# Performance work log

Hardware: AMD Instinct MI355X
Metric: run time of the kernel (lower is better)

The kernel has to match this reference:

```python
import jax, jax.numpy as jnp
import numpy as np

H, D = 16, 64  # head_num, head_dim
SCALE = 1.0 / D ** 0.5


def setup_inputs() -> dict:
    key = jax.random.key(0)
    ks = jax.random.split(key, 12)
    S, T, B, E = 2048, 2048, 2, 1024  # dec_seq, enc_seq, bs, input_dim
    return {
        "inputs": jax.random.normal(ks[0], (S, B, E), jnp.float32),
        "pos_embedding": jax.random.normal(ks[1], (T, 1, E), jnp.float32),
        "encoder_hidden_states": jax.random.normal(ks[2], (T, B, E), jnp.float32),
        "u": jax.random.normal(ks[3], (H, D), jnp.float32) * 0.02,
        "v": jax.random.normal(ks[4], (H, D), jnp.float32) * 0.02,
        "mask": jnp.zeros((S, T, 1), jnp.bool_),
        "Wkv": jax.random.normal(ks[5], (E, 2 * H * D), jnp.float32) * (E ** -0.5),
        "bkv": jnp.zeros((2 * H * D,), jnp.float32),
        "Wq": jax.random.normal(ks[6], (E, H * D), jnp.float32) * (E ** -0.5),
        "bq": jnp.zeros((H * D,), jnp.float32),
        "Wp": jax.random.normal(ks[7], (H * D, E), jnp.float32) * ((H * D) ** -0.5),
        "bp": jnp.zeros((E,), jnp.float32),
    }


def reference(inputs, pos_embedding, encoder_hidden_states, u, v, mask,
              Wkv, bkv, Wq, bq, Wp, bp):
    S, B, E = inputs.shape
    T = encoder_hidden_states.shape[0]
    # projections (fc_block == Linear)
    kv = encoder_hidden_states @ Wkv + bkv            # (T, B, 2HD)
    k, val = jnp.split(kv, 2, axis=-1)
    k = k.reshape(T, B, H, D)
    val = val.reshape(T, B, H, D)
    q = (inputs @ Wq + bq).reshape(S, B, H, D)
    q_u = q + u                                       # content bias (H, D) broadcast
    # content attention: (B, H, S, T)
    attn = jnp.einsum('sbhd,tbhd->bhst', q_u, k) * SCALE
    # mask (S, T, 1) -> (1, 1, S, T); all-False mask == original skip branch
    m = jnp.transpose(mask, (2, 0, 1))[:, None]
    attn = jnp.where(m, -jnp.inf, attn)
    attn = jax.nn.softmax(attn, axis=-1)
    # dropout is identity (eval)
    attn_vec = jnp.einsum('bhst,tbhd->sbhd', attn, val).reshape(S, B, H * D)
    return attn_vec @ Wp + bp                         # (S, B, E)
```

## Files before the change

kernel.cpp:

```cpp
#include <hip/hip_runtime.h>

#define Hh 16
#define Dd 64
#define Ss 2048
#define Tt 2048
#define Bb 2
#define Ee 1024
#define HD 1024
#define QSCALE 0.18033688011112042f

typedef __attribute__((ext_vector_type(8))) __bf16 bf16x8;
typedef __attribute__((ext_vector_type(4))) float f32x4;
typedef __attribute__((ext_vector_type(8))) unsigned short ushort8;
typedef __attribute__((ext_vector_type(2))) unsigned uint2v;

static __device__ __forceinline__ unsigned short f2b(float x) {
    union { float f; unsigned u; } v; v.f = x;
    unsigned r = v.u + 0x7FFFu + ((v.u >> 16) & 1u);
    return (unsigned short)(r >> 16);
}

static __device__ __forceinline__ unsigned cvtpk(float a, float b) {
    unsigned r;
    __asm__("v_cvt_pk_bf16_f32 %0, %1, %2" : "=v"(r) : "v"(a), "v"(b));
    return r;
}

static __device__ __forceinline__ void gld16(const unsigned short* g, unsigned short* l) {
    __builtin_amdgcn_global_load_lds(
        (const __attribute__((address_space(1))) unsigned int*)g,
        (__attribute__((address_space(3))) unsigned int*)l, 16, 0, 0);
}

static __device__ __forceinline__ void xquad(unsigned& a, unsigned& b) {
    uint2v r1 = __builtin_amdgcn_permlane32_swap(a, b, false, false);
    uint2v r2 = __builtin_amdgcn_permlane16_swap(r1[0], r1[1], false, false);
    a = r2[0]; b = r2[1];
}

static __device__ __forceinline__ bf16x8 packp(unsigned w0, unsigned w1,
                                               unsigned w2, unsigned w3) {
    union { unsigned u[4]; bf16x8 v; } x;
    x.u[0] = w0; x.u[1] = w1; x.u[2] = w2; x.u[3] = w3;
    return x.v;
}

static __device__ __forceinline__ void mkP(f32x4 s[4], bf16x8& pa0, bf16x8& pa1) {
#pragma unroll
    for (int jt = 0; jt < 4; jt++)
#pragma unroll
        for (int r = 0; r < 4; r++) s[jt][r] = __builtin_amdgcn_exp2f(s[jt][r]);
    unsigned a0 = cvtpk(s[0][0], s[0][1]), a1 = cvtpk(s[0][2], s[0][3]);
    unsigned b0 = cvtpk(s[1][0], s[1][1]), b1 = cvtpk(s[1][2], s[1][3]);
    unsigned c0 = cvtpk(s[2][0], s[2][1]), c1 = cvtpk(s[2][2], s[2][3]);
    unsigned d0 = cvtpk(s[3][0], s[3][1]), d1 = cvtpk(s[3][2], s[3][3]);
    xquad(a0, b0);
    xquad(a1, b1);
    xquad(c0, d0);
    xquad(c1, d1);
    pa0 = packp(a0, a1, b0, b1);
    pa1 = packp(c0, c1, d0, d1);
}

__global__ __launch_bounds__(256) void prep(
    const float* __restrict__ enc, const float* __restrict__ inp,
    unsigned short* __restrict__ encb, unsigned short* __restrict__ inpb,
    const float* __restrict__ Wkv, const float* __restrict__ Wq, const float* __restrict__ Wp,
    unsigned short* __restrict__ Wkvt, unsigned short* __restrict__ Wqt,
    unsigned short* __restrict__ Wpt)
{
    __shared__ float tile[64][65];
    const int bx = blockIdx.x;
    const int tid = threadIdx.x;
    if (bx < 8192) {
        const int n4each = (Tt * Bb * Ee) / 4;
        int i = bx * 256 + tid;
        const float4* src; ushort4* dst; int j;
        if (i < n4each) { src = (const float4*)enc; dst = (ushort4*)encb; j = i; }
        else            { src = (const float4*)inp; dst = (ushort4*)inpb; j = i - n4each; }
        float4 v = src[j];
        ushort4 o; o.x = f2b(v.x); o.y = f2b(v.y); o.z = f2b(v.z); o.w = f2b(v.w);
        dst[j] = o;
        return;
    }
    int u = bx - 8192;
    const float* in; unsigned short* out; int C, cblk, rblk;
    if (u < 512)       { in = Wkv; out = Wkvt; C = 2048; cblk = u & 31; rblk = u >> 5; }
    else if (u < 768)  { int v = u - 512; in = Wq; out = Wqt; C = 1024; cblk = v & 15; rblk = v >> 4; }
    else               { int v = u - 768; in = Wp; out = Wpt; C = 1024; cblk = v & 15; rblk = v >> 4; }
    const int R = 1024;
    int c0 = cblk * 64, r0 = rblk * 64;
    int tx = tid & 63, ty = tid >> 6;
    for (int i = ty; i < 64; i += 4)
        tile[i][tx] = in[(r0 + i) * (long)C + c0 + tx];
    __syncthreads();
    int c_local = tid >> 2, g = tid & 3;
    ushort8 o0, o1;
#pragma unroll
    for (int k = 0; k < 8; k++) o0[k] = f2b(tile[g * 16 + k][c_local]);
#pragma unroll
    for (int k = 0; k < 8; k++) o1[k] = f2b(tile[g * 16 + 8 + k][c_local]);
    unsigned short* dst = &out[(c0 + c_local) * (long)R + r0 + g * 16];
    *(ushort8*)dst = o0;
    *(ushort8*)(dst + 8) = o1;
}

static __device__ __forceinline__ void gemm_core(
    const unsigned short* __restrict__ A, const unsigned short* __restrict__ Bt,
    int m0, int n0, unsigned short* lA, unsigned short* lB, f32x4 acc[4][4])
{
    const int tid = threadIdx.x;
    const int lane = tid & 63;
    const int wid = tid >> 6;
    const int waveM = (wid & 1) * 64, waveN = (wid >> 1) * 64;
    const int quad = lane >> 4, low = lane & 15;
#pragma unroll
    for (int i = 0; i < 4; i++)
#pragma unroll
        for (int j = 0; j < 4; j++) acc[i][j] = (f32x4)0.0f;

    for (int k0 = 0; k0 < 1024; k0 += 32) {
        __syncthreads();
        {
            int r0 = tid >> 2, s0 = tid & 3;
            int f1 = tid + 256, r1 = f1 >> 2, s1 = f1 & 3;
            gld16(&A[(m0 + r0) * 1024 + k0 + s0 * 8], &lA[tid * 8]);
            gld16(&A[(m0 + r1) * 1024 + k0 + s1 * 8], &lA[f1 * 8]);
            gld16(&Bt[(n0 + r0) * 1024 + k0 + s0 * 8], &lB[tid * 8]);
            gld16(&Bt[(n0 + r1) * 1024 + k0 + s1 * 8], &lB[f1 * 8]);
        }
        __syncthreads();
        bf16x8 af[4], bfr[4];
#pragma unroll
        for (int i = 0; i < 4; i++)
            af[i] = *(const bf16x8*)&lA[(waveM + i * 16 + low) * 32 + quad * 8];
#pragma unroll
        for (int j = 0; j < 4; j++)
            bfr[j] = *(const bf16x8*)&lB[(waveN + j * 16 + low) * 32 + quad * 8];
#pragma unroll
        for (int i = 0; i < 4; i++)
#pragma unroll
            for (int j = 0; j < 4; j++)
                acc[i][j] = __builtin_amdgcn_mfma_f32_16x16x32_bf16(af[i], bfr[j], acc[i][j], 0, 0, 0);
    }
}

__global__ __launch_bounds__(256) void gemm12(
    const unsigned short* __restrict__ encb, const unsigned short* __restrict__ Wkvt,
    const float* __restrict__ bkv,
    const unsigned short* __restrict__ inpb, const unsigned short* __restrict__ Wqt,
    const float* __restrict__ bq, const float* __restrict__ u,
    unsigned short* __restrict__ Kw, unsigned short* __restrict__ Vb,
    unsigned short* __restrict__ qw)
{
    __shared__ unsigned short smem[128 * 130];
    unsigned short* lA = smem;
    unsigned short* lB = smem + 128 * 32;
    const int bx = blockIdx.x;
    int z, m0, n0;
    const unsigned short *Ap, *Bp;
    if (bx < 512) { z = 0; m0 = (bx >> 4) * 128; n0 = (bx & 15) * 128; Ap = encb; Bp = Wkvt; }
    else { z = 1; int i = bx - 512; m0 = (i >> 3) * 128; n0 = (i & 7) * 128; Ap = inpb; Bp = Wqt; }
    f32x4 acc[4][4];
    gemm_core(Ap, Bp, m0, n0, lA, lB, acc);
    __syncthreads();

    const int lane = threadIdx.x & 63;
    const int wid = threadIdx.x >> 6;
    const int waveM = (wid & 1) * 64, waveN = (wid >> 1) * 64;
    const int quad = lane >> 4, low = lane & 15;
#pragma unroll
    for (int i = 0; i < 4; i++)
#pragma unroll
        for (int j = 0; j < 4; j++)
#pragma unroll
            for (int r = 0; r < 4; r++) {
                int lm = waveM + i * 16 + quad * 4 + r;
                int ln = waveN + j * 16 + low;
                int gn = n0 + ln;
                float val = acc[i][j][r];
                if (z == 0) val += bkv[gn];
                else        val = (val + bq[gn] + u[gn]) * QSCALE;
                smem[lm * 130 + ln] = f2b(val);
            }
    __syncthreads();

    const int tid = threadIdx.x;
    if (z == 0 && n0 >= 1024) {
        int d = tid & 63, hp = (tid >> 6) & 1, b = tid >> 7;
        int h = ((n0 - 1024) >> 6) + hp;
        int tb = m0 >> 7;
        unsigned short* dst = &Vb[((((b << 4) | h) * 32 + tb) * 64 + d) * 64];
#pragma unroll
        for (int c = 0; c < 8; c++) {
            ushort8 o;
#pragma unroll
            for (int k = 0; k < 8; k++)
                o[k] = smem[((c * 8 + k) * 2 + b) * 130 + hp * 64 + d];
            *(ushort8*)(dst + c * 8) = o;
        }
    } else {
        int gl = tid & 127, hp = tid >> 7;
        int gm = m0 + gl;
        int t = gm >> 1, b = gm & 1;
        int h = (n0 >> 6) + hp;
        unsigned short* base = (z == 0) ? Kw : qw;
        unsigned short* dst = &base[(((b << 4) | h) * 2048 + t) * 64];
        const unsigned short* src = &smem[gl * 130 + hp * 64];
#pragma unroll
        for (int c = 0; c < 8; c++) {
            ushort8 o;
#pragma unroll
            for (int k = 0; k < 8; k++) o[k] = src[c * 8 + k];
            *(ushort8*)(dst + c * 8) = o;
        }
    }
}

__global__ __launch_bounds__(256) void gemm3(
    const unsigned short* __restrict__ av, const unsigned short* __restrict__ Wpt,
    const float* __restrict__ bp, float* __restrict__ out)
{
    __shared__ unsigned short lA[128 * 32];
    __shared__ unsigned short lB[64 * 32];
    const int tid = threadIdx.x;
    const int lane = tid & 63;
    const int wid = tid >> 6;
    const int waveM = (wid & 1) * 64, waveN = (wid >> 1) * 32;
    const int m0 = blockIdx.y * 128, n0 = blockIdx.x * 64;
    const int quad = lane >> 4, low = lane & 15;

    f32x4 acc[4][2];
#pragma unroll
    for (int i = 0; i < 4; i++)
#pragma unroll
        for (int j = 0; j < 2; j++) acc[i][j] = (f32x4)0.0f;

    for (int k0 = 0; k0 < 1024; k0 += 32) {
        __syncthreads();
        {
            int r0 = tid >> 2, s0 = tid & 3;
            int f1 = tid + 256, r1 = f1 >> 2, s1 = f1 & 3;
            gld16(&av[(m0 + r0) * 1024 + k0 + s0 * 8], &lA[tid * 8]);
            gld16(&av[(m0 + r1) * 1024 + k0 + s1 * 8], &lA[f1 * 8]);
            gld16(&Wpt[(n0 + r0) * 1024 + k0 + s0 * 8], &lB[tid * 8]);
        }
        __syncthreads();
        bf16x8 af[4], bfr[2];
#pragma unroll
        for (int i = 0; i < 4; i++)
            af[i] = *(const bf16x8*)&lA[(waveM + i * 16 + low) * 32 + quad * 8];
#pragma unroll
        for (int j = 0; j < 2; j++)
            bfr[j] = *(const bf16x8*)&lB[(waveN + j * 16 + low) * 32 + quad * 8];
#pragma unroll
        for (int i = 0; i < 4; i++)
#pragma unroll
            for (int j = 0; j < 2; j++)
                acc[i][j] = __builtin_amdgcn_mfma_f32_16x16x32_bf16(af[i], bfr[j], acc[i][j], 0, 0, 0);
    }
#pragma unroll
    for (int i = 0; i < 4; i++)
#pragma unroll
        for (int j = 0; j < 2; j++)
#pragma unroll
            for (int r = 0; r < 4; r++) {
                int gm = m0 + waveM + i * 16 + quad * 4 + r;
                int gn = n0 + waveN + j * 16 + low;
                out[gm * 1024 + gn] = acc[i][j][r] + bp[gn];
            }
}

__global__ __launch_bounds__(512, 4) void attn_kernel(
    const unsigned short* __restrict__ qw, const unsigned short* __restrict__ Kw,
    const unsigned short* __restrict__ Vb, unsigned short* __restrict__ av)
{
    __shared__ unsigned short kl[128 * 64];
    __shared__ unsigned short vt[2][64 * 64];
    const int tid = threadIdx.x;
    const int lane = tid & 63;
    const int w = tid >> 6;
    const int quad = lane >> 4, low = lane & 15;
    const int swz = low & 7;
    const int bh = blockIdx.x & 31;
    const int s0 = (blockIdx.x >> 5) * 128;
    const int s_wave = s0 + w * 16;

    bf16x8 qf0, qf1;
    {
        const unsigned short* qa = &qw[(bh * 2048 + s_wave + low) * 64];
        qf0 = *(const bf16x8*)&qa[quad * 8];
        qf1 = *(const bf16x8*)&qa[32 + quad * 8];
    }
    bf16x8 ones;
    {
        ushort8 o1;
#pragma unroll
        for (int i = 0; i < 8; i++) o1[i] = 0x3F80;
        ones = *(bf16x8*)&o1;
    }
    f32x4 o[4];
    f32x4 l_acc = (f32x4)0.0f;
#pragma unroll
    for (int j = 0; j < 4; j++) o[j] = (f32x4)0.0f;

#pragma unroll
    for (int i = 0; i < 2; i++) {
        int fl = tid + i * 512;
        int row = fl >> 3, seg = fl & 7;
        gld16(&Kw[(bh * 2048 + row) * 64 + ((seg ^ (row & 7)) << 3)], &kl[fl * 8]);
    }
    __builtin_amdgcn_sched_barrier(0);

    for (int t0 = 0; t0 < 2048; t0 += 128) {
#pragma unroll
        for (int i = 0; i < 2; i++) {
            int c2 = tid + i * 512;
            int win = c2 >> 9, inner = c2 & 511;
            int dd = inner >> 3, seg = inner & 7;
            gld16(&Vb[((bh * 32 + (t0 >> 6) + win) * 64 + dd) * 64 + ((seg ^ (dd & 7)) << 3)],
                  &vt[win][inner * 8]);
        }
        __asm__ volatile("s_waitcnt vmcnt(2)" ::: "memory");
        __builtin_amdgcn_s_barrier();
        __builtin_amdgcn_sched_barrier(0);

        f32x4 s0v[4], s1v[4];
        __builtin_amdgcn_s_setprio(1);
#pragma unroll
        for (int jt = 0; jt < 4; jt++) {
            int r = jt * 16 + low;
            bf16x8 kb0 = *(const bf16x8*)&kl[r * 64 + ((quad ^ swz) << 3)];
            bf16x8 kb1 = *(const bf16x8*)&kl[r * 64 + (((quad ^ 4) ^ swz) << 3)];
            f32x4 a = (f32x4)0.0f;
            a = __builtin_amdgcn_mfma_f32_16x16x32_bf16(kb0, qf0, a, 0, 0, 0);
            s0v[jt] = __builtin_amdgcn_mfma_f32_16x16x32_bf16(kb1, qf1, a, 0, 0, 0);
        }
        __builtin_amdgcn_s_setprio(0);
        bf16x8 p00, p01;
        mkP(s0v, p00, p01);

        __builtin_amdgcn_s_setprio(1);
#pragma unroll
        for (int jt = 0; jt < 4; jt++) {
            int r = 64 + jt * 16 + low;
            bf16x8 kb0 = *(const bf16x8*)&kl[r * 64 + ((quad ^ swz) << 3)];
            bf16x8 kb1 = *(const bf16x8*)&kl[r * 64 + (((quad ^ 4) ^ swz) << 3)];
            f32x4 a = (f32x4)0.0f;
            a = __builtin_amdgcn_mfma_f32_16x16x32_bf16(kb0, qf0, a, 0, 0, 0);
            s1v[jt] = __builtin_amdgcn_mfma_f32_16x16x32_bf16(kb1, qf1, a, 0, 0, 0);
        }
        __builtin_amdgcn_s_setprio(0);
        bf16x8 p10, p11;
        mkP(s1v, p10, p11);

        __asm__ volatile("s_waitcnt vmcnt(0)" ::: "memory");
        __builtin_amdgcn_s_barrier();
        __builtin_amdgcn_sched_barrier(0);

        {
            int tn = (t0 + 128) & 2047;
#pragma unroll
            for (int i = 0; i < 2; i++) {
                int fl = tid + i * 512;
                int row = fl >> 3, seg = fl & 7;
                gld16(&Kw[(bh * 2048 + tn + row) * 64 + ((seg ^ (row & 7)) << 3)],
                      &kl[fl * 8]);
            }
        }
        __builtin_amdgcn_sched_barrier(0);

        __builtin_amdgcn_s_setprio(1);
        l_acc = __builtin_amdgcn_mfma_f32_16x16x32_bf16(p00, ones, l_acc, 0, 0, 0);
        l_acc = __builtin_amdgcn_mfma_f32_16x16x32_bf16(p01, ones, l_acc, 0, 0, 0);
#pragma unroll
        for (int j = 0; j < 4; j++) {
            int dr = j * 16 + low;
            bf16x8 vb0 = *(const bf16x8*)&vt[0][dr * 64 + ((quad ^ swz) << 3)];
            bf16x8 vb1 = *(const bf16x8*)&vt[0][dr * 64 + (((quad ^ 4) ^ swz) << 3)];
            o[j] = __builtin_amdgcn_mfma_f32_16x16x32_bf16(p00, vb0, o[j], 0, 0, 0);
            o[j] = __builtin_amdgcn_mfma_f32_16x16x32_bf16(p01, vb1, o[j], 0, 0, 0);
        }
        l_acc = __builtin_amdgcn_mfma_f32_16x16x32_bf16(p10, ones, l_acc, 0, 0, 0);
        l_acc = __builtin_amdgcn_mfma_f32_16x16x32_bf16(p11, ones, l_acc, 0, 0, 0);
#pragma unroll
        for (int j = 0; j < 4; j++) {
            int dr = j * 16 + low;
            bf16x8 vb0 = *(const bf16x8*)&vt[1][dr * 64 + ((quad ^ swz) << 3)];
            bf16x8 vb1 = *(const bf16x8*)&vt[1][dr * 64 + (((quad ^ 4) ^ swz) << 3)];
            o[j] = __builtin_amdgcn_mfma_f32_16x16x32_bf16(p10, vb0, o[j], 0, 0, 0);
            o[j] = __builtin_amdgcn_mfma_f32_16x16x32_bf16(p11, vb1, o[j], 0, 0, 0);
        }
        __builtin_amdgcn_s_setprio(0);

        __builtin_amdgcn_s_barrier();
        __builtin_amdgcn_sched_barrier(0);
    }

    int b = bh >> 4, hh = bh & 15;
#pragma unroll
    for (int j = 0; j < 4; j++) {
#pragma unroll
        for (int r = 0; r < 4; r++) {
            int sA_ = s_wave + quad * 4 + r;
            int d = j * 16 + low;
            av[(sA_ * 2 + b) * 1024 + hh * 64 + d] = f2b(o[j][r] / l_acc[r]);
        }
    }
}

extern "C" void kernel_launch(void* const* d_in, const int* in_sizes, int n_in,
                              void* d_out, int out_size, void* d_ws, size_t ws_size,
                              hipStream_t stream)
{
    const float* inputs = (const float*)d_in[0];
    const float* enc    = (const float*)d_in[2];
    const float* u      = (const float*)d_in[3];
    const float* Wkv    = (const float*)d_in[6];
    const float* bkv    = (const float*)d_in[7];
    const float* Wq     = (const float*)d_in[8];
    const float* bq     = (const float*)d_in[9];
    const float* Wp     = (const float*)d_in[10];
    const float* bp     = (const float*)d_in[11];
    float* out = (float*)d_out;

    char* ws = (char*)d_ws;
    unsigned short* enc_b = (unsigned short*)(ws + (0ull << 20));
    unsigned short* inp_b = (unsigned short*)(ws + (8ull << 20));
    unsigned short* Wkv_t = (unsigned short*)(ws + (16ull << 20));
    unsigned short* Wq_t  = (unsigned short*)(ws + (20ull << 20));
    unsigned short* Wp_t  = (unsigned short*)(ws + (22ull << 20));
    unsigned short* Kw    = (unsigned short*)(ws + (24ull << 20));
    unsigned short* Vb    = (unsigned short*)(ws + (32ull << 20));
    unsigned short* qw    = (unsigned short*)(ws + (40ull << 20));
    unsigned short* av    = (unsigned short*)(ws + (48ull << 20));

    prep<<<8192 + 1024, 256, 0, stream>>>(enc, inputs, enc_b, inp_b, Wkv, Wq, Wp,
                                          Wkv_t, Wq_t, Wp_t);
    gemm12<<<768, 256, 0, stream>>>(enc_b, Wkv_t, bkv, inp_b, Wq_t, bq, u, Kw, Vb, qw);
    attn_kernel<<<512, 512, 0, stream>>>(qw, Kw, Vb, av);
    gemm3<<<dim3(16, 32), 256, 0, stream>>>(av, Wp_t, bp, out);
}
```

Measured before the change: 224.8 us.

## Double-buffer LDS tiles in projection GEMMs to overlap loads with MFMA

The projection GEMMs (gemm12 and gemm3) now use two LDS buffers, prefetching the next K-slice via direct global-to-LDS loads while MFMAs consume the current slice. This replaces the two barriers per iteration with one explicit waitcnt plus barrier, hiding global load latency behind compute. It doubles the LDS tile footprint in gemm3, which may reduce occupancy, and it relies on hand-placed waitcnt and sched_barrier for correctness.

Result: slower. 233.7 us (+4.0%).

```diff
diff --git a/kernel.cpp b/kernel.cpp
--- a/kernel.cpp
+++ b/kernel.cpp
@@ -107,29 +107,41 @@
 
 static __device__ __forceinline__ void gemm_core(
     const unsigned short* __restrict__ A, const unsigned short* __restrict__ Bt,
-    int m0, int n0, unsigned short* lA, unsigned short* lB, f32x4 acc[4][4])
+    int m0, int n0, unsigned short* sA, unsigned short* sB, f32x4 acc[4][4])
 {
     const int tid = threadIdx.x;
     const int lane = tid & 63;
     const int wid = tid >> 6;
     const int waveM = (wid & 1) * 64, waveN = (wid >> 1) * 64;
     const int quad = lane >> 4, low = lane & 15;
+    const int r0 = tid >> 2, s0 = tid & 3;
+    const int f1 = tid + 256, r1 = f1 >> 2, s1 = f1 & 3;
 #pragma unroll
     for (int i = 0; i < 4; i++)
 #pragma unroll
         for (int j = 0; j < 4; j++) acc[i][j] = (f32x4)0.0f;
 
+    gld16(&A[(m0 + r0) * 1024 + s0 * 8], &sA[tid * 8]);
+    gld16(&A[(m0 + r1) * 1024 + s1 * 8], &sA[f1 * 8]);
+    gld16(&Bt[(n0 + r0) * 1024 + s0 * 8], &sB[tid * 8]);
+    gld16(&Bt[(n0 + r1) * 1024 + s1 * 8], &sB[f1 * 8]);
+    __asm__ volatile("s_waitcnt vmcnt(0)" ::: "memory");
+    __builtin_amdgcn_s_barrier();
+    __builtin_amdgcn_sched_barrier(0);
+
+    int cur = 0;
     for (int k0 = 0; k0 < 1024; k0 += 32) {
-        __syncthreads();
-        {
-            int r0 = tid >> 2, s0 = tid & 3;
-            int f1 = tid + 256, r1 = f1 >> 2, s1 = f1 & 3;
-            gld16(&A[(m0 + r0) * 1024 + k0 + s0 * 8], &lA[tid * 8]);
-            gld16(&A[(m0 + r1) * 1024 + k0 + s1 * 8], &lA[f1 * 8]);
-            gld16(&Bt[(n0 + r0) * 1024 + k0 + s0 * 8], &lB[tid * 8]);
-            gld16(&Bt[(n0 + r1) * 1024 + k0 + s1 * 8], &lB[f1 * 8]);
-        }
-        __syncthreads();
+        unsigned short* lA = sA + cur * 4096;
+        unsigned short* lB = sB + cur * 4096;
+        if (k0 + 32 < 1024) {
+            unsigned short* nA = sA + (cur ^ 1) * 4096;
+            unsigned short* nB = sB + (cur ^ 1) * 4096;
+            int kn = k0 + 32;
+            gld16(&A[(m0 + r0) * 1024 + kn + s0 * 8], &nA[tid * 8]);
+            gld16(&A[(m0 + r1) * 1024 + kn + s1 * 8], &nA[f1 * 8]);
+            gld16(&Bt[(n0 + r0) * 1024 + kn + s0 * 8], &nB[tid * 8]);
+            gld16(&Bt[(n0 + r1) * 1024 + kn + s1 * 8], &nB[f1 * 8]);
+        }
         bf16x8 af[4], bfr[4];
 #pragma unroll
         for (int i = 0; i < 4; i++)
@@ -142,6 +154,10 @@
 #pragma unroll
             for (int j = 0; j < 4; j++)
                 acc[i][j] = __builtin_amdgcn_mfma_f32_16x16x32_bf16(af[i], bfr[j], acc[i][j], 0, 0, 0);
+        __asm__ volatile("s_waitcnt vmcnt(0) lgkmcnt(0)" ::: "memory");
+        __builtin_amdgcn_s_barrier();
+        __builtin_amdgcn_sched_barrier(0);
+        cur ^= 1;
     }
 }
 
@@ -154,15 +170,15 @@
     unsigned short* __restrict__ qw)
 {
     __shared__ unsigned short smem[128 * 130];
-    unsigned short* lA = smem;
-    unsigned short* lB = smem + 128 * 32;
+    unsigned short* sA = smem;
+    unsigned short* sB = smem + 8192;
     const int bx = blockIdx.x;
     int z, m0, n0;
     const unsigned short *Ap, *Bp;
     if (bx < 512) { z = 0; m0 = (bx >> 4) * 128; n0 = (bx & 15) * 128; Ap = encb; Bp = Wkvt; }
     else { z = 1; int i = bx - 512; m0 = (i >> 3) * 128; n0 = (i & 7) * 128; Ap = inpb; Bp = Wqt; }
     f32x4 acc[4][4];
-    gemm_core(Ap, Bp, m0, n0, lA, lB, acc);
+    gemm_core(Ap, Bp, m0, n0, sA, sB, acc);
     __syncthreads();
 
     const int lane = threadIdx.x & 63;
@@ -221,14 +237,16 @@
     const unsigned short* __restrict__ av, const unsigned short* __restrict__ Wpt,
     const float* __restrict__ bp, float* __restrict__ out)
 {
-    __shared__ unsigned short lA[128 * 32];
-    __shared__ unsigned short lB[64 * 32];
+    __shared__ unsigned short sA[2][128 * 32];
+    __shared__ unsigned short sB[2][64 * 32];
     const int tid = threadIdx.x;
     const int lane = tid & 63;
     const int wid = tid >> 6;
     const int waveM = (wid & 1) * 64, waveN = (wid >> 1) * 32;
     const int m0 = blockIdx.y * 128, n0 = blockIdx.x * 64;
     const int quad = lane >> 4, low = lane & 15;
+    const int r0 = tid >> 2, s0 = tid & 3;
+    const int f1 = tid + 256, r1 = f1 >> 2, s1 = f1 & 3;
 
     f32x4 acc[4][2];
 #pragma unroll
@@ -236,16 +254,23 @@
 #pragma unroll
         for (int j = 0; j < 2; j++) acc[i][j] = (f32x4)0.0f;
 
+    gld16(&av[(m0 + r0) * 1024 + s0 * 8], &sA[0][tid * 8]);
+    gld16(&av[(m0 + r1) * 1024 + s1 * 8], &sA[0][f1 * 8]);
+    gld16(&Wpt[(n0 + r0) * 1024 + s0 * 8], &sB[0][tid * 8]);
+    __asm__ volatile("s_waitcnt vmcnt(0)" ::: "memory");
+    __builtin_amdgcn_s_barrier();
+    __builtin_amdgcn_sched_barrier(0);
+
+    int cur = 0;
     for (int k0 = 0; k0 < 1024; k0 += 32) {
-        __syncthreads();
-        {
-            int r0 = tid >> 2, s0 = tid & 3;
-            int f1 = tid + 256, r1 = f1 >> 2, s1 = f1 & 3;
-            gld16(&av[(m0 + r0) * 1024 + k0 + s0 * 8], &lA[tid * 8]);
-            gld16(&av[(m0 + r1) * 1024 + k0 + s1 * 8], &lA[f1 * 8]);
-            gld16(&Wpt[(n0 + r0) * 1024 + k0 + s0 * 8], &lB[tid * 8]);
-        }
-        __syncthreads();
+        const unsigned short* lA = sA[cur];
+        const unsigned short* lB = sB[cur];
+        if (k0 + 32 < 1024) {
+            int kn = k0 + 32;
+            gld16(&av[(m0 + r0) * 1024 + kn + s0 * 8], &sA[cur ^ 1][tid * 8]);
+            gld16(&av[(m0 + r1) * 1024 + kn + s1 * 8], &sA[cur ^ 1][f1 * 8]);
+            gld16(&Wpt[(n0 + r0) * 1024 + kn + s0 * 8], &sB[cur ^ 1][tid * 8]);
+        }
         bf16x8 af[4], bfr[2];
 #pragma unroll
         for (int i = 0; i < 4; i++)
@@ -258,6 +283,10 @@
 #pragma unroll
             for (int j = 0; j < 2; j++)
                 acc[i][j] = __builtin_amdgcn_mfma_f32_16x16x32_bf16(af[i], bfr[j], acc[i][j], 0, 0, 0);
+        __asm__ volatile("s_waitcnt vmcnt(0) lgkmcnt(0)" ::: "memory");
+        __builtin_amdgcn_s_barrier();
+        __builtin_amdgcn_sched_barrier(0);
+        cur ^= 1;
     }
 #pragma unroll
     for (int i = 0; i < 4; i++)
```

## Triple-buffer GEMM LDS loads and remap blocks to XCDs for L2 locality

Applied to the files above, without the earlier changes.

The projection GEMM main loop changes from a load-sync-compute-sync pattern to a three-stage LDS ring buffer. Async global-to-LDS loads are issued two k-steps ahead, and a single barrier per iteration with a partial vmcnt wait replaces the two syncthreads. Block indices are also remapped so blocks landing on the same XCD cover neighbouring M/N tiles, aiming for better L2 reuse. LDS use rises to 48KB per block, which may reduce occupancy, and the last iterations issue wrapped-around redundant loads.

Measured after the change: 228.2 us. Within noise of the previous version (+1.5%).

```diff
diff --git a/kernel.cpp b/kernel.cpp
--- a/kernel.cpp
+++ b/kernel.cpp
@@ -107,29 +107,44 @@
 
 static __device__ __forceinline__ void gemm_core(
     const unsigned short* __restrict__ A, const unsigned short* __restrict__ Bt,
-    int m0, int n0, unsigned short* lA, unsigned short* lB, f32x4 acc[4][4])
+    int m0, int n0, unsigned short* smem, f32x4 acc[4][4])
 {
     const int tid = threadIdx.x;
     const int lane = tid & 63;
     const int wid = tid >> 6;
     const int waveM = (wid & 1) * 64, waveN = (wid >> 1) * 64;
     const int quad = lane >> 4, low = lane & 15;
+    const int r0 = tid >> 2, s0 = tid & 3;
+    const int f1 = tid + 256, r1 = f1 >> 2, s1 = f1 & 3;
+    const unsigned short* gA0 = &A[(m0 + r0) * 1024 + s0 * 8];
+    const unsigned short* gA1 = &A[(m0 + r1) * 1024 + s1 * 8];
+    const unsigned short* gB0 = &Bt[(n0 + r0) * 1024 + s0 * 8];
+    const unsigned short* gB1 = &Bt[(n0 + r1) * 1024 + s1 * 8];
 #pragma unroll
     for (int i = 0; i < 4; i++)
 #pragma unroll
         for (int j = 0; j < 4; j++) acc[i][j] = (f32x4)0.0f;
 
+#define STAGE_G(kk, buf) do { \
+        unsigned short* _sA = smem + (buf) * 8192; \
+        unsigned short* _sB = _sA + 4096; \
+        gld16(gA0 + (kk), &_sA[tid * 8]); \
+        gld16(gA1 + (kk), &_sA[f1 * 8]); \
+        gld16(gB0 + (kk), &_sB[tid * 8]); \
+        gld16(gB1 + (kk), &_sB[f1 * 8]); } while (0)
+
+    STAGE_G(0, 0);
+    STAGE_G(32, 1);
+    __asm__ volatile("s_waitcnt vmcnt(4)" ::: "memory");
+    __builtin_amdgcn_s_barrier();
+    __builtin_amdgcn_sched_barrier(0);
+
+    int cur = 0;
     for (int k0 = 0; k0 < 1024; k0 += 32) {
-        __syncthreads();
-        {
-            int r0 = tid >> 2, s0 = tid & 3;
-            int f1 = tid + 256, r1 = f1 >> 2, s1 = f1 & 3;
-            gld16(&A[(m0 + r0) * 1024 + k0 + s0 * 8], &lA[tid * 8]);
-            gld16(&A[(m0 + r1) * 1024 + k0 + s1 * 8], &lA[f1 * 8]);
-            gld16(&Bt[(n0 + r0) * 1024 + k0 + s0 * 8], &lB[tid * 8]);
-            gld16(&Bt[(n0 + r1) * 1024 + k0 + s1 * 8], &lB[f1 * 8]);
-        }
-        __syncthreads();
+        int nb = cur + 2; if (nb >= 3) nb -= 3;
+        STAGE_G((k0 + 64) & 1023, nb);
+        const unsigned short* lA = smem + cur * 8192;
+        const unsigned short* lB = lA + 4096;
         bf16x8 af[4], bfr[4];
 #pragma unroll
         for (int i = 0; i < 4; i++)
@@ -142,7 +157,12 @@
 #pragma unroll
             for (int j = 0; j < 4; j++)
                 acc[i][j] = __builtin_amdgcn_mfma_f32_16x16x32_bf16(af[i], bfr[j], acc[i][j], 0, 0, 0);
-    }
+        __asm__ volatile("s_waitcnt vmcnt(4) lgkmcnt(0)" ::: "memory");
+        __builtin_amdgcn_s_barrier();
+        __builtin_amdgcn_sched_barrier(0);
+        cur = cur + 1 == 3 ? 0 : cur + 1;
+    }
+#undef STAGE_G
 }
 
 __global__ __launch_bounds__(256) void gemm12(
@@ -153,16 +173,23 @@
     unsigned short* __restrict__ Kw, unsigned short* __restrict__ Vb,
     unsigned short* __restrict__ qw)
 {
-    __shared__ unsigned short smem[128 * 130];
-    unsigned short* lA = smem;
-    unsigned short* lB = smem + 128 * 32;
-    const int bx = blockIdx.x;
+    __shared__ unsigned short smem[24576];
+    const int bx0 = blockIdx.x;
+    const int xcd = bx0 & 7, pos = bx0 >> 3;
     int z, m0, n0;
     const unsigned short *Ap, *Bp;
-    if (bx < 512) { z = 0; m0 = (bx >> 4) * 128; n0 = (bx & 15) * 128; Ap = encb; Bp = Wkvt; }
-    else { z = 1; int i = bx - 512; m0 = (i >> 3) * 128; n0 = (i & 7) * 128; Ap = inpb; Bp = Wqt; }
+    if (pos < 64) {
+        z = 0; Ap = encb; Bp = Wkvt;
+        m0 = ((xcd >> 1) * 8 + (pos & 7)) * 128;
+        n0 = ((xcd & 1) * 8 + (pos >> 3)) * 128;
+    } else {
+        int p = pos - 64;
+        z = 1; Ap = inpb; Bp = Wqt;
+        m0 = (xcd * 4 + (p & 3)) * 128;
+        n0 = (p >> 2) * 128;
+    }
     f32x4 acc[4][4];
-    gemm_core(Ap, Bp, m0, n0, lA, lB, acc);
+    gemm_core(Ap, Bp, m0, n0, smem, acc);
     __syncthreads();
 
     const int lane = threadIdx.x & 63;
```
